# Performance work log

Measured on AMD Instinct MI355X. Metric: run time of the kernel, lower is better.

Reference implementation:

```python
import jax, jax.numpy as jnp
import numpy as np

EMB = 512
LIN = 64
ATT = 64
H = 8
EPS = 1e-6


def layer_norm(x, eps=EPS):
    # layer norm over last dim, no affine params (matches F.layer_norm w/o weight/bias)
    mu = jnp.mean(x, axis=-1, keepdims=True)
    var = jnp.var(x, axis=-1, keepdims=True)
    return (x - mu) * jax.lax.rsqrt(var + eps)


def setup_inputs() -> dict:
    key = jax.random.key(0)
    k1, k2, k3, k4, k5 = jax.random.split(key, 5)
    B, N = 8, 2048
    x = jax.random.normal(k1, (B, N, EMB), dtype=jnp.float32)
    rel_pos_bias = jax.random.normal(k2, (H, N, N), dtype=jnp.float32)
    invalid_attn_mask = jnp.ones((B, N, N), dtype=jnp.float32)
    uvqk = jax.random.normal(k3, (EMB, LIN * 2 * H + ATT * H * 2), dtype=jnp.float32) * 0.02
    o_w = jax.random.normal(k4, (EMB, LIN * H), dtype=jnp.float32) * (1.0 / np.sqrt(LIN * H))
    o_b = jnp.zeros((EMB,), dtype=jnp.float32)
    return {"x": x, "rel_pos_bias": rel_pos_bias, "invalid_attn_mask": invalid_attn_mask,
            "uvqk": uvqk, "o_w": o_w, "o_b": o_b}


def reference(x, rel_pos_bias, invalid_attn_mask, uvqk, o_w, o_b):
    B, N, D = x.shape
    residual = x
    normed = layer_norm(x)                                   # [B,N,D]
    proj = jax.nn.silu(jnp.einsum('bnd,de->bne', normed, uvqk))  # [B,N,2*LIN*H+2*ATT*H]
    lh = LIN * H
    ah = ATT * H
    u = proj[..., :lh]                                        # [B,N,LIN*H]
    v = proj[..., lh:2 * lh].reshape(B, N, H, LIN)            # [B,N,H,LIN]
    q = proj[..., 2 * lh:2 * lh + ah].reshape(B, N, H, ATT)
    k = proj[..., 2 * lh + ah:].reshape(B, N, H, ATT)
    qk = jnp.einsum('bnhd,bmhd->bhnm', q, k) + rel_pos_bias[None]  # [B,H,N,N]
    qk = jax.nn.silu(qk) * invalid_attn_mask[:, None]
    attn = jnp.einsum('bhnm,bmhd->bnhd', qk, v).reshape(B, N, lh)
    gated = u * layer_norm(attn)
    out = jnp.einsum('bnf,ef->bne', gated, o_w) + o_b          # dropout off (eval)
    return residual + out
```

## Files before the change

### kernel.cpp

```cpp
#include <hip/hip_runtime.h>
#include <stdint.h>

typedef short bf16x8   __attribute__((ext_vector_type(8)));
typedef short short4v  __attribute__((ext_vector_type(4)));
typedef short short8v  __attribute__((ext_vector_type(8)));
typedef float f32x4    __attribute__((ext_vector_type(4)));

typedef __attribute__((address_space(3))) uint32_t lds_u32;
typedef const __attribute__((address_space(1))) uint32_t glob_u32;

__device__ __forceinline__ void gl_lds16(const void* g, void* l) {
  __builtin_amdgcn_global_load_lds((glob_u32*)g, (lds_u32*)l, 16, 0, 0);
}

__device__ __forceinline__ float bf2f(short u) {
  union { float f; uint32_t i; } v; v.i = ((uint32_t)(uint16_t)u) << 16; return v.f;
}
__device__ __forceinline__ short f2bf(float f) {
  union { float f; uint32_t i; } v; v.f = f;
  uint32_t r = v.i + 0x7FFFu + ((v.i >> 16) & 1u);
  return (short)(r >> 16);
}
__device__ __forceinline__ float siluf(float x) {
  return x * __builtin_amdgcn_rcpf(1.0f + __expf(-x));
}
__device__ __forceinline__ f32x4 mfma16(bf16x8 a, bf16x8 b, f32x4 c) {
  return __builtin_amdgcn_mfma_f32_16x16x32_bf16(a, b, c, 0, 0, 0);
}

__global__ __launch_bounds__(256) void k_ln(const float* __restrict__ x, short* __restrict__ xn) {
  int row = blockIdx.x * 4 + (threadIdx.x >> 6);
  int lane = threadIdx.x & 63;
  const float4* xr = (const float4*)(x + (size_t)row * 512);
  float4 a = xr[lane * 2], b = xr[lane * 2 + 1];
  float s  = a.x + a.y + a.z + a.w + b.x + b.y + b.z + b.w;
  float s2 = a.x*a.x + a.y*a.y + a.z*a.z + a.w*a.w + b.x*b.x + b.y*b.y + b.z*b.z + b.w*b.w;
#pragma unroll
  for (int m = 1; m < 64; m <<= 1) { s += __shfl_xor(s, m); s2 += __shfl_xor(s2, m); }
  float mu = s * (1.f / 512.f);
  float rstd = rsqrtf(s2 * (1.f / 512.f) - mu * mu + 1e-6f);
  float v[8] = {a.x, a.y, a.z, a.w, b.x, b.y, b.z, b.w};
  short8v o;
#pragma unroll
  for (int j = 0; j < 8; ++j) o[j] = f2bf((v[j] - mu) * rstd);
  *(short8v*)&xn[(size_t)row * 512 + lane * 8] = o;
}

__global__ __launch_bounds__(256) void k_prep_w(const float* __restrict__ uvqk, short* __restrict__ Wt) {
  __shared__ float t[64][65];
  int k0 = blockIdx.x * 64;
  int c0 = blockIdx.y * 64;
  for (int i = threadIdx.x; i < 64 * 64; i += 256) {
    int r = i >> 6, c = i & 63;
    t[r][c] = uvqk[(size_t)(k0 + r) * 2048 + c0 + c];
  }
  __syncthreads();
  for (int i = threadIdx.x; i < 64 * 64; i += 256) {
    int c = i >> 6, k = i & 63;
    Wt[(size_t)(c0 + c) * 512 + k0 + k] = f2bf(t[k][c]);
  }
}

__global__ __launch_bounds__(256) void k_cast_ow(const float* __restrict__ ow, short* __restrict__ owt) {
  int i = blockIdx.x * 256 + threadIdx.x;
  owt[i] = f2bf(ow[i]);
}

__device__ __forceinline__ void gemm_core(const short* __restrict__ A, const short* __restrict__ Bt,
                                          int t0, int c0, short* As, short* Bs, f32x4 (&acc)[4][4]) {
  int tid = threadIdx.x;
  int w = tid >> 6, lane = tid & 63, l16 = lane & 15, lq = lane >> 4;
  int wm = (w >> 1) * 64, wn = (w & 1) * 64;
  int srow = tid >> 3;
  int sch = (tid & 7) ^ (srow & 7);
  const short* ag = A  + (size_t)(t0 + srow) * 512 + sch * 8;
  const short* bg = Bt + (size_t)(c0 + srow) * 512 + sch * 8;

  for (int k0 = 0; k0 < 512; k0 += 64) {
#pragma unroll
    for (int j = 0; j < 4; ++j) {
      gl_lds16(ag + (size_t)j * 32 * 512 + k0, (char*)As + j * 4096 + w * 1024);
      gl_lds16(bg + (size_t)j * 32 * 512 + k0, (char*)Bs + j * 4096 + w * 1024);
    }
    asm volatile("s_waitcnt vmcnt(0)" ::: "memory");
    __syncthreads();
#pragma unroll
    for (int kk = 0; kk < 2; ++kk) {
      bf16x8 af[4], bf[4];
#pragma unroll
      for (int mi = 0; mi < 4; ++mi) {
        int row = wm + mi * 16 + l16;
        af[mi] = *(const bf16x8*)&As[row * 64 + (((kk * 4 + lq) ^ (l16 & 7)) * 8)];
      }
#pragma unroll
      for (int ni = 0; ni < 4; ++ni) {
        int row = wn + ni * 16 + l16;
        bf[ni] = *(const bf16x8*)&Bs[row * 64 + (((kk * 4 + lq) ^ (l16 & 7)) * 8)];
      }
#pragma unroll
      for (int mi = 0; mi < 4; ++mi)
#pragma unroll
        for (int ni = 0; ni < 4; ++ni)
          acc[mi][ni] = mfma16(af[mi], bf[ni], acc[mi][ni]);
    }
    __syncthreads();
  }
}

__global__ __launch_bounds__(256) void k_gemm1(const short* __restrict__ A, const short* __restrict__ Bt,
                                               short* __restrict__ proj, short* __restrict__ Vt) {
  __shared__ short As[128 * 64], Bs[128 * 64];
  int c0 = blockIdx.x * 128, t0 = blockIdx.y * 128;
  f32x4 acc[4][4] = {};
  gemm_core(A, Bt, t0, c0, As, Bs, acc);
  int tid = threadIdx.x, w = tid >> 6, lane = tid & 63, l16 = lane & 15, lq = lane >> 4;
  int wm = (w >> 1) * 64, wn = (w & 1) * 64;
  bool isv = (c0 >= 512 && c0 < 1024);
#pragma unroll
  for (int mi = 0; mi < 4; ++mi)
#pragma unroll
    for (int ni = 0; ni < 4; ++ni) {
      int c = c0 + wn + ni * 16 + l16;
      int trow = t0 + wm + mi * 16 + lq * 4;
      if (isv) {
        int hh = (c - 512) >> 6, d = (c - 512) & 63;
        int bb = trow >> 11, nn = trow & 2047;
        short4v pv;
#pragma unroll
        for (int i = 0; i < 4; ++i) pv[i] = f2bf(siluf(acc[mi][ni][i]));
        *(short4v*)&Vt[((size_t)(bb * 8 + hh) * 64 + d) * 2048 + nn] = pv;
      } else {
#pragma unroll
        for (int i = 0; i < 4; ++i)
          proj[(size_t)(trow + i) * 2048 + c] = f2bf(siluf(acc[mi][ni][i]));
      }
    }
}

__global__ __launch_bounds__(256) void k_attn(const short* __restrict__ proj,
                                              const short* __restrict__ Vt,
                                              const float* __restrict__ rpb,
                                              const float* __restrict__ maskp,
                                              float* __restrict__ attn) {
  __shared__ __align__(16) short Ks[64 * 64];
  __shared__ __align__(16) short Vs[64 * 64];
  __shared__ __align__(16) float Sr[128 * 68];
  __shared__ __align__(16) short Ps[128 * 64];

  int p = blockIdx.x;
  int L = (p & 7) * 128 + (p >> 3);
  int qt = L >> 6, h = (L >> 3) & 7, b = L & 7;
  int n0 = qt * 128;

  int tid = threadIdx.x;
  int w = tid >> 6, lane = tid & 63, l16 = lane & 15, lq = lane >> 4;

  bf16x8 qf[2][2];
#pragma unroll
  for (int mi = 0; mi < 2; ++mi)
#pragma unroll
    for (int kk = 0; kk < 2; ++kk) {
      int n = n0 + w * 32 + mi * 16 + l16;
      qf[mi][kk] = *(const bf16x8*)&proj[(size_t)(b * 2048 + n) * 2048 + 1024 + h * 64 + kk * 32 + lq * 8];
    }

  int j8 = lane >> 3, c8 = lane & 7;
  int srcc = (c8 ^ j8) * 8;
  const short* kg = proj + (size_t)(b * 2048) * 2048 + 1536 + h * 64 + srcc;
  const short* vg = Vt + (size_t)((b * 8 + h) * 64) * 2048 + srcc;

  int er = tid >> 4, ec = tid & 15;
  const float* rpb_p = rpb + (size_t)h * 4194304 + (size_t)(n0 + er) * 2048 + ec * 4;
  const float* msk_p = maskp + (size_t)b * 4194304 + (size_t)(n0 + er) * 2048 + ec * 4;

  f32x4 acc_o[2][4] = {};

  for (int kv0 = 0; kv0 < 2048; kv0 += 64) {
    __builtin_amdgcn_s_barrier();
#pragma unroll
    for (int j = 0; j < 2; ++j)
      gl_lds16(kg + (size_t)(kv0 + w * 16 + j * 8 + j8) * 2048, Ks + w * 1024 + j * 512);
#pragma unroll
    for (int j = 0; j < 2; ++j)
      gl_lds16(vg + (size_t)(w * 16 + j * 8 + j8) * 2048 + kv0, Vs + w * 1024 + j * 512);
    __builtin_amdgcn_sched_barrier(0);
    float4 rv[8], mv[8];
#pragma unroll
    for (int jj = 0; jj < 8; ++jj) {
      rv[jj] = *(const float4*)(rpb_p + (size_t)jj * 32768 + kv0);
      mv[jj] = *(const float4*)(msk_p + (size_t)jj * 32768 + kv0);
    }
    __builtin_amdgcn_sched_barrier(0);
    asm volatile("s_waitcnt vmcnt(16)" ::: "memory");
    __builtin_amdgcn_s_barrier();

    f32x4 s[2][4] = {};
#pragma unroll
    for (int kk = 0; kk < 2; ++kk) {
      bf16x8 kf[4];
#pragma unroll
      for (int ni = 0; ni < 4; ++ni)
        kf[ni] = *(const bf16x8*)&Ks[(ni * 16 + l16) * 64 + (((kk * 4 + lq) ^ (l16 & 7)) * 8)];
#pragma unroll
      for (int mi = 0; mi < 2; ++mi)
#pragma unroll
        for (int ni = 0; ni < 4; ++ni)
          s[mi][ni] = mfma16(qf[mi][kk], kf[ni], s[mi][ni]);
    }
#pragma unroll
    for (int mi = 0; mi < 2; ++mi)
#pragma unroll
      for (int ni = 0; ni < 4; ++ni)
#pragma unroll
        for (int i = 0; i < 4; ++i)
          Sr[(w * 32 + mi * 16 + lq * 4 + i) * 68 + ni * 16 + l16] = s[mi][ni][i];
    asm volatile("s_waitcnt lgkmcnt(0)" ::: "memory");
    __builtin_amdgcn_s_barrier();

#pragma unroll
    for (int jj = 0; jj < 8; ++jj) {
      int r = jj * 16 + er;
      f32x4 sv = *(const f32x4*)&Sr[r * 68 + ec * 4];
      float xr[4] = {rv[jj].x, rv[jj].y, rv[jj].z, rv[jj].w};
      float xm[4] = {mv[jj].x, mv[jj].y, mv[jj].z, mv[jj].w};
      short4v pk;
#pragma unroll
      for (int e = 0; e < 4; ++e) {
        float xx = sv[e] + xr[e];
        pk[e] = f2bf(siluf(xx) * xm[e]);
      }
      *(short4v*)((char*)Ps + r * 128 + (((ec >> 1) ^ (r & 7)) * 16) + (ec & 1) * 8) = pk;
    }
    asm volatile("s_waitcnt lgkmcnt(0)" ::: "memory");
    __builtin_amdgcn_s_barrier();

#pragma unroll
    for (int ks = 0; ks < 2; ++ks) {
      bf16x8 pf[2], vf[4];
#pragma unroll
      for (int mi = 0; mi < 2; ++mi) {
        int rp = w * 32 + mi * 16 + l16;
        pf[mi] = *(const bf16x8*)((const char*)Ps + rp * 128 + (((ks * 4 + lq) ^ (rp & 7)) * 16));
      }
#pragma unroll
      for (int ni = 0; ni < 4; ++ni)
        vf[ni] = *(const bf16x8*)&Vs[(ni * 16 + l16) * 64 + (((ks * 4 + lq) ^ (l16 & 7)) * 8)];
#pragma unroll
      for (int mi = 0; mi < 2; ++mi)
#pragma unroll
        for (int ni = 0; ni < 4; ++ni)
          acc_o[mi][ni] = mfma16(pf[mi], vf[ni], acc_o[mi][ni]);
    }
  }

#pragma unroll
  for (int mi = 0; mi < 2; ++mi)
#pragma unroll
    for (int ni = 0; ni < 4; ++ni)
#pragma unroll
      for (int i = 0; i < 4; ++i) {
        int n = n0 + w * 32 + mi * 16 + lq * 4 + i;
        attn[(size_t)(b * 2048 + n) * 512 + h * 64 + ni * 16 + l16] = acc_o[mi][ni][i];
      }
}

__global__ __launch_bounds__(256) void k_gate(const float* __restrict__ attn, const short* __restrict__ proj,
                                              short* __restrict__ gated) {
  int row = blockIdx.x * 4 + (threadIdx.x >> 6);
  int lane = threadIdx.x & 63;
  const float4* ar = (const float4*)(attn + (size_t)row * 512);
  float4 a = ar[lane * 2], b = ar[lane * 2 + 1];
  float s  = a.x + a.y + a.z + a.w + b.x + b.y + b.z + b.w;
  float s2 = a.x*a.x + a.y*a.y + a.z*a.z + a.w*a.w + b.x*b.x + b.y*b.y + b.z*b.z + b.w*b.w;
#pragma unroll
  for (int m = 1; m < 64; m <<= 1) { s += __shfl_xor(s, m); s2 += __shfl_xor(s2, m); }
  float mu = s * (1.f / 512.f);
  float rstd = rsqrtf(s2 * (1.f / 512.f) - mu * mu + 1e-6f);
  float v[8] = {a.x, a.y, a.z, a.w, b.x, b.y, b.z, b.w};
  short8v u = *(const short8v*)&proj[(size_t)row * 2048 + lane * 8];
  short8v g;
#pragma unroll
  for (int j = 0; j < 8; ++j) g[j] = f2bf(bf2f(u[j]) * ((v[j] - mu) * rstd));
  *(short8v*)&gated[(size_t)row * 512 + lane * 8] = g;
}

__global__ __launch_bounds__(256) void k_gemm2(const short* __restrict__ A, const short* __restrict__ Bt,
                                               const float* __restrict__ ob, const float* __restrict__ x,
                                               float* __restrict__ out) {
  __shared__ short As[128 * 64], Bs[128 * 64];
  int c0 = blockIdx.x * 128, t0 = blockIdx.y * 128;
  f32x4 acc[4][4] = {};
  gemm_core(A, Bt, t0, c0, As, Bs, acc);
  int tid = threadIdx.x, w = tid >> 6, lane = tid & 63, l16 = lane & 15, lq = lane >> 4;
  int wm = (w >> 1) * 64, wn = (w & 1) * 64;
#pragma unroll
  for (int mi = 0; mi < 4; ++mi)
#pragma unroll
    for (int ni = 0; ni < 4; ++ni) {
      int e = c0 + wn + ni * 16 + l16;
      float bias = ob[e];
#pragma unroll
      for (int i = 0; i < 4; ++i) {
        int t = t0 + wm + mi * 16 + lq * 4 + i;
        out[(size_t)t * 512 + e] = acc[mi][ni][i] + bias + x[(size_t)t * 512 + e];
      }
    }
}

extern "C" void kernel_launch(void* const* d_in, const int* in_sizes, int n_in,
                              void* d_out, int out_size, void* d_ws, size_t ws_size,
                              hipStream_t stream) {
  const float* x    = (const float*)d_in[0];
  const float* rpb  = (const float*)d_in[1];
  const float* mask = (const float*)d_in[2];
  const float* uvqk = (const float*)d_in[3];
  const float* o_w  = (const float*)d_in[4];
  const float* o_b  = (const float*)d_in[5];
  float* out = (float*)d_out;

  char* p = (char*)d_ws;
  short* xn   = (short*)p; p += 16384ull * 512 * 2;
  short* Wt   = (short*)p; p += 2048ull * 512 * 2;
  short* owt  = (short*)p; p += 512ull * 512 * 2;
  short* proj = (short*)p; p += 16384ull * 2048 * 2;
  short* Vt   = (short*)p; p += 8ull * 8 * 64 * 2048 * 2;
  float* attn = (float*)p; p += 16384ull * 512 * 4;
  short* gated = xn;

  k_ln    <<<4096, 256, 0, stream>>>(x, xn);
  k_prep_w<<<dim3(8, 32), 256, 0, stream>>>(uvqk, Wt);
  k_cast_ow<<<1024, 256, 0, stream>>>(o_w, owt);
  k_gemm1 <<<dim3(16, 128), 256, 0, stream>>>(xn, Wt, proj, Vt);
  k_attn  <<<1024, 256, 0, stream>>>(proj, Vt, rpb, mask, attn);
  k_gate  <<<4096, 256, 0, stream>>>(attn, proj, gated);
  k_gemm2 <<<dim3(4, 128), 256, 0, stream>>>(gated, owt, o_b, x, out);
}
```

Before: 364.9 us.

## Double-buffer K/V tiles and apply bias/mask directly in MFMA register layout

The attention kernel now double-buffers the K and V tiles in LDS and prefetches the next tile while the current one is computed, so each iteration needs one barrier instead of three. The fp32 score staging buffer is removed: rel-pos bias and mask values are loaded per lane to match the MFMA accumulator layout, and SiLU plus the bf16 pack are applied in registers before writing P. Launch bounds now request 3 blocks per CU. The trade-off is that bias and mask are read as scalar 4-byte loads instead of float4 vectors, and these dominant HBM reads are no longer issued as early in each iteration.

Result: slower. 443.4 us (+21.5%).

```diff
diff --git a/kernel.cpp b/kernel.cpp
--- a/kernel.cpp
+++ b/kernel.cpp
@@ -137,14 +137,13 @@
     }
 }
 
-__global__ __launch_bounds__(256) void k_attn(const short* __restrict__ proj,
-                                              const short* __restrict__ Vt,
-                                              const float* __restrict__ rpb,
-                                              const float* __restrict__ maskp,
-                                              float* __restrict__ attn) {
-  __shared__ __align__(16) short Ks[64 * 64];
-  __shared__ __align__(16) short Vs[64 * 64];
-  __shared__ __align__(16) float Sr[128 * 68];
+__global__ __launch_bounds__(256, 3) void k_attn(const short* __restrict__ proj,
+                                                 const short* __restrict__ Vt,
+                                                 const float* __restrict__ rpb,
+                                                 const float* __restrict__ maskp,
+                                                 float* __restrict__ attn) {
+  __shared__ __align__(16) short Ks[2][64 * 64];
+  __shared__ __align__(16) short Vs[2][64 * 64];
   __shared__ __align__(16) short Ps[128 * 64];
 
   int p = blockIdx.x;
@@ -169,30 +168,43 @@
   const short* kg = proj + (size_t)(b * 2048) * 2048 + 1536 + h * 64 + srcc;
   const short* vg = Vt + (size_t)((b * 8 + h) * 64) * 2048 + srcc;
 
-  int er = tid >> 4, ec = tid & 15;
-  const float* rpb_p = rpb + (size_t)h * 4194304 + (size_t)(n0 + er) * 2048 + ec * 4;
-  const float* msk_p = maskp + (size_t)b * 4194304 + (size_t)(n0 + er) * 2048 + ec * 4;
+  const float* rp_t = rpb   + (size_t)h * 4194304 + (size_t)(n0 + w * 32 + lq * 4) * 2048 + l16;
+  const float* mk_t = maskp + (size_t)b * 4194304 + (size_t)(n0 + w * 32 + lq * 4) * 2048 + l16;
 
   f32x4 acc_o[2][4] = {};
 
-  for (int kv0 = 0; kv0 < 2048; kv0 += 64) {
-    __builtin_amdgcn_s_barrier();
-#pragma unroll
-    for (int j = 0; j < 2; ++j)
-      gl_lds16(kg + (size_t)(kv0 + w * 16 + j * 8 + j8) * 2048, Ks + w * 1024 + j * 512);
-#pragma unroll
-    for (int j = 0; j < 2; ++j)
-      gl_lds16(vg + (size_t)(w * 16 + j * 8 + j8) * 2048 + kv0, Vs + w * 1024 + j * 512);
-    __builtin_amdgcn_sched_barrier(0);
-    float4 rv[8], mv[8];
-#pragma unroll
-    for (int jj = 0; jj < 8; ++jj) {
-      rv[jj] = *(const float4*)(rpb_p + (size_t)jj * 32768 + kv0);
-      mv[jj] = *(const float4*)(msk_p + (size_t)jj * 32768 + kv0);
-    }
-    __builtin_amdgcn_sched_barrier(0);
-    asm volatile("s_waitcnt vmcnt(16)" ::: "memory");
-    __builtin_amdgcn_s_barrier();
+#pragma unroll
+  for (int j = 0; j < 2; ++j) {
+    gl_lds16(kg + (size_t)(w * 16 + j * 8 + j8) * 2048, &Ks[0][w * 1024 + j * 512]);
+    gl_lds16(vg + (size_t)(w * 16 + j * 8 + j8) * 2048, &Vs[0][w * 1024 + j * 512]);
+  }
+  asm volatile("s_waitcnt vmcnt(0)" ::: "memory");
+  __builtin_amdgcn_s_barrier();
+
+  for (int t = 0; t < 32; ++t) {
+    int kv0 = t << 6;
+    const short* Kc = Ks[t & 1];
+    const short* Vc = Vs[t & 1];
+    short* Kn = Ks[(t & 1) ^ 1];
+    short* Vn = Vs[(t & 1) ^ 1];
+    int kvn = (kv0 + 64) & 2047;
+
+#pragma unroll
+    for (int j = 0; j < 2; ++j) {
+      gl_lds16(kg + (size_t)(kvn + w * 16 + j * 8 + j8) * 2048, &Kn[w * 1024 + j * 512]);
+      gl_lds16(vg + (size_t)(w * 16 + j * 8 + j8) * 2048 + kvn, &Vn[w * 1024 + j * 512]);
+    }
+
+    const float* rp_i = rp_t + kv0;
+    const float* mk_i = mk_t + kv0;
+    float rv0[4][4], mv0[4][4];
+#pragma unroll
+    for (int ni = 0; ni < 4; ++ni)
+#pragma unroll
+      for (int i = 0; i < 4; ++i) {
+        rv0[ni][i] = rp_i[(size_t)i * 2048 + ni * 16];
+        mv0[ni][i] = mk_i[(size_t)i * 2048 + ni * 16];
+      }
 
     f32x4 s[2][4] = {};
 #pragma unroll
@@ -200,39 +212,43 @@
       bf16x8 kf[4];
 #pragma unroll
       for (int ni = 0; ni < 4; ++ni)
-        kf[ni] = *(const bf16x8*)&Ks[(ni * 16 + l16) * 64 + (((kk * 4 + lq) ^ (l16 & 7)) * 8)];
+        kf[ni] = *(const bf16x8*)&Kc[(ni * 16 + l16) * 64 + (((kk * 4 + lq) ^ (l16 & 7)) * 8)];
 #pragma unroll
       for (int mi = 0; mi < 2; ++mi)
 #pragma unroll
         for (int ni = 0; ni < 4; ++ni)
           s[mi][ni] = mfma16(qf[mi][kk], kf[ni], s[mi][ni]);
     }
-#pragma unroll
-    for (int mi = 0; mi < 2; ++mi)
-#pragma unroll
-      for (int ni = 0; ni < 4; ++ni)
-#pragma unroll
-        for (int i = 0; i < 4; ++i)
-          Sr[(w * 32 + mi * 16 + lq * 4 + i) * 68 + ni * 16 + l16] = s[mi][ni][i];
-    asm volatile("s_waitcnt lgkmcnt(0)" ::: "memory");
-    __builtin_amdgcn_s_barrier();
-
-#pragma unroll
-    for (int jj = 0; jj < 8; ++jj) {
-      int r = jj * 16 + er;
-      f32x4 sv = *(const f32x4*)&Sr[r * 68 + ec * 4];
-      float xr[4] = {rv[jj].x, rv[jj].y, rv[jj].z, rv[jj].w};
-      float xm[4] = {mv[jj].x, mv[jj].y, mv[jj].z, mv[jj].w};
-      short4v pk;
-#pragma unroll
-      for (int e = 0; e < 4; ++e) {
-        float xx = sv[e] + xr[e];
-        pk[e] = f2bf(siluf(xx) * xm[e]);
-      }
-      *(short4v*)((char*)Ps + r * 128 + (((ec >> 1) ^ (r & 7)) * 16) + (ec & 1) * 8) = pk;
-    }
-    asm volatile("s_waitcnt lgkmcnt(0)" ::: "memory");
-    __builtin_amdgcn_s_barrier();
+
+    float rv1[4][4], mv1[4][4];
+#pragma unroll
+    for (int ni = 0; ni < 4; ++ni)
+#pragma unroll
+      for (int i = 0; i < 4; ++i) {
+        rv1[ni][i] = rp_i[(size_t)(16 + i) * 2048 + ni * 16];
+        mv1[ni][i] = mk_i[(size_t)(16 + i) * 2048 + ni * 16];
+      }
+
+#pragma unroll
+    for (int ni = 0; ni < 4; ++ni)
+#pragma unroll
+      for (int i = 0; i < 4; ++i) {
+        float xx = s[0][ni][i] + rv0[ni][i];
+        float pv = siluf(xx) * mv0[ni][i];
+        int row = w * 32 + lq * 4 + i;
+        int cb = ni * 2 + (l16 >> 3);
+        *(short*)((char*)Ps + row * 128 + (((cb ^ (row & 7)) << 4) + (l16 & 7) * 2)) = f2bf(pv);
+      }
+#pragma unroll
+    for (int ni = 0; ni < 4; ++ni)
+#pragma unroll
+      for (int i = 0; i < 4; ++i) {
+        float xx = s[1][ni][i] + rv1[ni][i];
+        float pv = siluf(xx) * mv1[ni][i];
+        int row = w * 32 + 16 + lq * 4 + i;
+        int cb = ni * 2 + (l16 >> 3);
+        *(short*)((char*)Ps + row * 128 + (((cb ^ (row & 7)) << 4) + (l16 & 7) * 2)) = f2bf(pv);
+      }
 
 #pragma unroll
     for (int ks = 0; ks < 2; ++ks) {
@@ -244,13 +260,16 @@
       }
 #pragma unroll
       for (int ni = 0; ni < 4; ++ni)
-        vf[ni] = *(const bf16x8*)&Vs[(ni * 16 + l16) * 64 + (((ks * 4 + lq) ^ (l16 & 7)) * 8)];
+        vf[ni] = *(const bf16x8*)&Vc[(ni * 16 + l16) * 64 + (((ks * 4 + lq) ^ (l16 & 7)) * 8)];
 #pragma unroll
       for (int mi = 0; mi < 2; ++mi)
 #pragma unroll
         for (int ni = 0; ni < 4; ++ni)
           acc_o[mi][ni] = mfma16(pf[mi], vf[ni], acc_o[mi][ni]);
     }
+
+    asm volatile("s_waitcnt vmcnt(0)" ::: "memory");
+    __builtin_amdgcn_s_barrier();
   }
 
 #pragma unroll
```
